# Performance work log

Hardware: AMD Instinct MI355X
Metric: run time of the kernel (lower is better)

Reference implementation:

```python
import jax, jax.numpy as jnp
import numpy as np

DIM = 512
NUM_HEADS = 8


def setup_inputs() -> dict:
    key = jax.random.key(0)
    ks = jax.random.split(key, 10)
    B, N, C = 2, 4096, DIM
    s = 0.02
    return {
        "x": jax.random.normal(ks[0], (B, N, C), dtype=jnp.float32),
        "Wq": jax.random.normal(ks[1], (C, C), dtype=jnp.float32) * s,
        "Wk": jax.random.normal(ks[2], (C, C), dtype=jnp.float32) * s,
        "Wv": jax.random.normal(ks[3], (C, C), dtype=jnp.float32) * s,
        "Wattn": jax.random.normal(ks[4], (C, C), dtype=jnp.float32) * s,
        "Wconv": jax.random.normal(ks[5], (C, C), dtype=jnp.float32) * s,
        "dw_kernel": jax.random.normal(ks[6], (C, 1, 3), dtype=jnp.float32) * s,  # depthwise (O, I/groups, K)
        "dw_bias": jax.random.normal(ks[7], (C,), dtype=jnp.float32) * s,
        "Wcout": jax.random.normal(ks[8], (C, C), dtype=jnp.float32) * s,
        "H": 8,
        "W": 512,
    }


def reference(x, Wq, Wk, Wv, Wattn, Wconv, dw_kernel, dw_bias, Wcout, H, W):
    B, N, C = x.shape
    nh = NUM_HEADS
    hd = C // nh
    scale = hd ** (-0.5)

    # QKV projections (torch Linear: x @ W.T), split heads -> [B, nh, N, hd]
    q = (x @ Wq.T).reshape(B, N, nh, hd).transpose(0, 2, 1, 3)
    k = (x @ Wk.T).reshape(B, N, nh, hd).transpose(0, 2, 1, 3)
    v = (x @ Wv.T).reshape(B, N, nh, hd).transpose(0, 2, 1, 3)

    # Materialized N x N attention (faithful to source)
    scores = jnp.einsum("bhqd,bhkd->bhqk", q, k) * scale
    weights = jax.nn.softmax(scores, axis=-1)
    attn = jnp.einsum("bhqk,bhkd->bhqd", weights, v)
    attn = attn.transpose(0, 2, 1, 3).reshape(B, N, C)
    attn_out = attn @ Wattn.T

    # Parallel depthwise-conv branch
    ci = (x @ Wconv.T).transpose(0, 2, 1)  # [B, C, N]
    co = jax.lax.conv_general_dilated(
        ci, dw_kernel,
        window_strides=(1,), padding=((1, 1),),
        feature_group_count=C,
        dimension_numbers=("NCH", "OIH", "NCH"),
    ) + dw_bias[None, :, None]
    conv_out = co.transpose(0, 2, 1) @ Wcout.T  # [B, N, C]

    out = attn_out + conv_out
    # NOTE: source shadows arg H with num_heads before the view
    return out.reshape(B, nh, W, C)
```

## Files before the change

kernel.cpp:

```cpp
#include <hip/hip_runtime.h>

typedef __attribute__((ext_vector_type(8))) short bf16x8;
typedef __attribute__((ext_vector_type(4))) float f32x4;

constexpr int kB = 2, kN = 4096, kC = 512, kNH = 8, kHD = 64;
constexpr int kBN = kB * kN;
constexpr int kWElems = 262144;
constexpr int kWAll = 6 * kWElems;
constexpr int kWExtra = 3584;
constexpr float kQScale = 0.1803368801f;

__device__ __forceinline__ short f2bf(float f) {
  union { float f; unsigned u; } v; v.f = f;
  unsigned r = v.u + 0x7fffu + ((v.u >> 16) & 1u);
  return (short)(r >> 16);
}
__device__ __forceinline__ float bf2f(short s) {
  union { unsigned u; float f; } v; v.u = ((unsigned)(unsigned short)s) << 16;
  return v.f;
}
__device__ __forceinline__ float exp2_(float x) {
#if __has_builtin(__builtin_amdgcn_exp2f)
  return __builtin_amdgcn_exp2f(x);
#else
  return exp2f(x);
#endif
}
__device__ __forceinline__ unsigned pk2bf(float a, float b) {
  union { float f; unsigned u; } ua, ub; ua.f = a; ub.f = b;
#if __has_builtin(__builtin_amdgcn_perm)
  return __builtin_amdgcn_perm(ub.u + 0x8000u, ua.u + 0x8000u, 0x07060302u);
#else
  return ((ua.u + 0x8000u) >> 16) | (((ub.u + 0x8000u) >> 16) << 16);
#endif
}

__device__ __forceinline__ bf16x8 ld8(const short* p) { return *(const bf16x8*)p; }
__device__ __forceinline__ bf16x8 ld8(const float* p) {
  float4 a = *(const float4*)p;
  float4 b = *(const float4*)(p + 4);
  bf16x8 r;
  r[0] = f2bf(a.x); r[1] = f2bf(a.y); r[2] = f2bf(a.z); r[3] = f2bf(a.w);
  r[4] = f2bf(b.x); r[5] = f2bf(b.y); r[6] = f2bf(b.z); r[7] = f2bf(b.w);
  return r;
}
__device__ __forceinline__ void stf(short* p, float v) { *p = f2bf(v); }
__device__ __forceinline__ void stf(float* p, float v) { *p = v; }

__device__ __forceinline__ void gload_lds16(const void* g, void* l) {
  __builtin_amdgcn_global_load_lds(
      (const __attribute__((address_space(1))) void*)g,
      (__attribute__((address_space(3))) void*)l, 16, 0, 0);
}

__global__ void detect_dtype(const unsigned* __restrict__ x, int* __restrict__ flag) {
  const int lane = threadIdx.x & 63;
  unsigned w = x[lane];
  int e = (int)((w >> 7) & 0xffu);
  bool bf = (e >= 100 && e <= 140);
  unsigned long long m = __ballot(bf);
  if (lane == 0) *flag = (__popcll(m) >= 32) ? 1 : 0;
}

constexpr int kW8 = kWAll / 8;
constexpr int kX8 = kBN * kC / 8;
__global__ __launch_bounds__(256) void convert_all(
    const void* Wq, const void* Wk, const void* Wv, const void* Wc,
    const void* Wa, const void* Wco, const void* dwk, const void* dwb,
    const void* x, const int* __restrict__ flag, short* __restrict__ dst,
    short* __restrict__ xb) {
  const int gtid = blockIdx.x * 256 + threadIdx.x;
  const bool bf = (*flag != 0);
  if (gtid < kW8) {
    const int e = gtid * 8;
    const int t = e >> 18, off = e & (kWElems - 1);
    const void* src = (t == 0) ? Wq : (t == 1) ? Wk : (t == 2) ? Wv
                    : (t == 3) ? Wc : (t == 4) ? Wa : Wco;
    bf16x8 v = bf ? ld8((const short*)src + off) : ld8((const float*)src + off);
    *(bf16x8*)(dst + e) = v;
  } else if (gtid < kW8 + kWExtra) {
    const int eoff = gtid - kW8;
    if (eoff < 1536) {
      dst[kWAll + eoff] = bf ? ((const short*)dwk)[eoff]
                             : f2bf(((const float*)dwk)[eoff]);
    } else if (eoff < 2048) {
      const int i = eoff - 1536;
      dst[kWAll + 1536 + i] = bf ? ((const short*)dwb)[i]
                                 : f2bf(((const float*)dwb)[i]);
    } else {
      const int t2 = eoff - 2048;
      const int tap = t2 >> 9, c = t2 & 511;
      dst[kWAll + 2048 + t2] = bf ? ((const short*)dwk)[c * 3 + tap]
                                  : f2bf(((const float*)dwk)[c * 3 + tap]);
    }
  } else if (gtid < kW8 + kWExtra + kX8) {
    const int e = (gtid - kW8 - kWExtra) * 8;
    bf16x8 v = bf ? ld8((const short*)x + e) : ld8((const float*)x + e);
    *(bf16x8*)(xb + e) = v;
  }
}

__global__ __launch_bounds__(256, 3) void proj_gemm(
    const short* __restrict__ xb, const short* __restrict__ wb,
    short* __restrict__ q, short* __restrict__ k, short* __restrict__ vT,
    short* __restrict__ ci) {
  __shared__ __align__(16) short As[128 * 64];
  __shared__ __align__(16) short Bs[128 * 64];
  const int t = threadIdx.x;
  const int wave = t >> 6, lane = t & 63;
  const int row = lane & 15, quad = lane >> 4;
  const int bn = blockIdx.x & 15;
  const int bm = blockIdx.x >> 4;
  const int m0 = bm * 128, n0 = bn * 128;
  const int wm = wave & 1, wn = wave >> 1;
  const int lrow = lane >> 3, lch = lane & 7;

  f32x4 acc[4][4];
#pragma unroll
  for (int mi = 0; mi < 4; ++mi)
#pragma unroll
    for (int ni = 0; ni < 4; ++ni)
#pragma unroll
      for (int r = 0; r < 4; ++r) acc[mi][ni][r] = 0.0f;

  for (int k0 = 0; k0 < kC; k0 += 64) {
#pragma unroll
    for (int p = 0; p < 4; ++p) {
      const int m = wave * 32 + p * 8 + lrow;
      const int kch = lch ^ (m & 7);
      gload_lds16(xb + (size_t)(m0 + m) * kC + k0 + kch * 8,
                  &As[(wave * 32 + p * 8) * 64]);
      gload_lds16(wb + (size_t)(n0 + m) * kC + k0 + kch * 8,
                  &Bs[(wave * 32 + p * 8) * 64]);
    }
    __syncthreads();

#pragma unroll
    for (int kk2 = 0; kk2 < 2; ++kk2) {
      bf16x8 af[4], bfr[4];
#pragma unroll
      for (int mi = 0; mi < 4; ++mi) {
        const int m = wm * 64 + mi * 16 + row;
        const int ch = (kk2 * 4 + quad) ^ (m & 7);
        af[mi] = *(const bf16x8*)(&As[m * 64 + ch * 8]);
      }
#pragma unroll
      for (int ni = 0; ni < 4; ++ni) {
        const int n = wn * 64 + ni * 16 + row;
        const int ch = (kk2 * 4 + quad) ^ (n & 7);
        bfr[ni] = *(const bf16x8*)(&Bs[n * 64 + ch * 8]);
      }
#pragma unroll
      for (int mi = 0; mi < 4; ++mi)
#pragma unroll
        for (int ni = 0; ni < 4; ++ni)
          acc[mi][ni] = __builtin_amdgcn_mfma_f32_16x16x32_bf16(
              af[mi], bfr[ni], acc[mi][ni], 0, 0, 0);
    }
    __syncthreads();
  }

  const int gc0 = n0 + wn * 64;
  const int mat = gc0 >> 9;
  const float scale = (mat == 0) ? kQScale : 1.0f;
#pragma unroll
  for (int mi = 0; mi < 4; ++mi) {
#pragma unroll
    for (int ni = 0; ni < 4; ++ni) {
#pragma unroll
      for (int r = 0; r < 4; ++r) {
        const int gm = m0 + wm * 64 + mi * 16 + quad * 4 + r;
        const int c_ = ((gc0 + ni * 16) & 511) + row;
        const int b_ = gm >> 12;
        const int n_ = gm & (kN - 1);
        const short bv = f2bf(acc[mi][ni][r] * scale);
        if (mat == 3) {
          ci[(b_ * kN + n_) * kC + c_] = bv;
        } else {
          const int h = c_ >> 6, d = c_ & 63;
          const int bh = b_ * kNH + h;
          if (mat == 0)      q[(bh * kN + n_) * kHD + d] = bv;
          else if (mat == 1) k[(bh * kN + n_) * kHD + d] = bv;
          else               vT[(bh * kHD + d) * kN + n_] = bv;
        }
      }
    }
  }
}

__global__ __launch_bounds__(256) void dwconv(
    const short* __restrict__ ci, const short* __restrict__ wb,
    short* __restrict__ cb) {
  const int e0 = (blockIdx.x * 256 + threadIdx.x) * 8;
  const int c0 = e0 & (kC - 1);
  const int bn = e0 >> 9;
  const int n_ = bn & (kN - 1);
  bf16x8 xc = ld8(ci + e0);
  bf16x8 xm, xp;
  if (n_ > 0) xm = ld8(ci + e0 - kC);
  else
#pragma unroll
    for (int i = 0; i < 8; ++i) xm[i] = 0;
  if (n_ < kN - 1) xp = ld8(ci + e0 + kC);
  else
#pragma unroll
    for (int i = 0; i < 8; ++i) xp[i] = 0;
  bf16x8 w0 = ld8(wb + kWAll + 2048 + c0);
  bf16x8 w1 = ld8(wb + kWAll + 2048 + 512 + c0);
  bf16x8 w2 = ld8(wb + kWAll + 2048 + 1024 + c0);
  bf16x8 bi = ld8(wb + kWAll + 1536 + c0);
  bf16x8 o;
#pragma unroll
  for (int i = 0; i < 8; ++i) {
    float a = bf2f(bi[i]) + bf2f(xm[i]) * bf2f(w0[i]) +
              bf2f(xc[i]) * bf2f(w1[i]) + bf2f(xp[i]) * bf2f(w2[i]);
    o[i] = f2bf(a);
  }
  *(bf16x8*)(cb + e0) = o;
}

__global__ __launch_bounds__(512, 4) void attn_flash(
    const short* __restrict__ q, const short* __restrict__ k,
    const short* __restrict__ vT, short* __restrict__ attn) {
  __shared__ __align__(16) short Kb[2][2][64 * 64];
  __shared__ __align__(16) short VbS[2][2][64 * 72];
  const int t = threadIdx.x;
  const int wave = t >> 6;
  const int lane = t & 63;
  const int row = lane & 15;
  const int quad = lane >> 4;
  const int qg = wave & 3;
  const int ks = wave >> 2;

  const int slot = blockIdx.x & 7;
  const int inner = blockIdx.x >> 3;
  const int bh = slot * 2 + (inner & 1);
  const int q0 = (inner >> 1) * 128 + qg * 32;

  const short* qbase = q + (size_t)(bh * kN + q0) * kHD;
  const short* kbase = k + (size_t)bh * kN * kHD;
  const short* vbase = vT + (size_t)bh * kHD * kN;

  bf16x8 qb[2][2];
#pragma unroll
  for (int g = 0; g < 2; ++g) {
    qb[g][0] = *(const bf16x8*)(qbase + (g * 16 + row) * kHD + quad * 8);
    qb[g][1] = *(const bf16x8*)(qbase + (g * 16 + row) * kHD + 32 + quad * 8);
  }

  f32x4 o[2][4];
#pragma unroll
  for (int g = 0; g < 2; ++g)
#pragma unroll
    for (int j = 0; j < 4; ++j)
#pragma unroll
      for (int r = 0; r < 4; ++r) o[g][j][r] = 0.0f;
  float l_[2] = {0.0f, 0.0f};

  const int ksrow = lane >> 3;
  const int kschunk = (lane & 7) ^ ksrow;
  auto stage_k = [&](int buf, int kt) {
#pragma unroll
    for (int s2 = 0; s2 < 2; ++s2)
      gload_lds16(
          kbase + (size_t)(s2 * 2048 + kt * 64 + wave * 8 + ksrow) * 64 +
              kschunk * 8,
          &Kb[buf][s2][wave * 512]);
  };

  const int sv = t >> 8;
  const int ii = t & 255;
  const int i0 = ii, i1 = ii + 256;
  const int sr0 = i0 >> 3, sc0 = i0 & 7;
  const int sr1 = i1 >> 3, sc1 = i1 & 7;
  const int vb0 = (sc0 >> 2) * 32 + (sc0 & 1) * 16 + (sc0 & 2) * 2;
  const int vb1 = (sc1 >> 2) * 32 + (sc1 & 1) * 16 + (sc1 & 2) * 2;

  auto stage_v = [&](int buf, bf16x8 v0, bf16x8 v1) {
    *(short4*)(&VbS[buf][sv][sr0 * 72 + vb0]) =
        make_short4(v0[0], v0[1], v0[2], v0[3]);
    *(short4*)(&VbS[buf][sv][sr0 * 72 + vb0 + 8]) =
        make_short4(v0[4], v0[5], v0[6], v0[7]);
    *(short4*)(&VbS[buf][sv][sr1 * 72 + vb1]) =
        make_short4(v1[0], v1[1], v1[2], v1[3]);
    *(short4*)(&VbS[buf][sv][sr1 * 72 + vb1 + 8]) =
        make_short4(v1[4], v1[5], v1[6], v1[7]);
  };

  const int c0s = ((quad) ^ (row & 7)) * 8;
  const int c1s = ((quad + 4) ^ (row & 7)) * 8;

  auto tile_step = [&](const short* kt_base, const short* vt_base) {
    f32x4 s[2][4];
#pragma unroll
    for (int g = 0; g < 2; ++g)
#pragma unroll
      for (int jk = 0; jk < 4; ++jk)
#pragma unroll
        for (int r = 0; r < 4; ++r) s[g][jk][r] = 0.0f;
    __builtin_amdgcn_s_setprio(1);
#pragma unroll
    for (int jk = 0; jk < 4; ++jk) {
      const short* kr = kt_base + (jk * 16 + row) * 64;
      bf16x8 a0 = *(const bf16x8*)(kr + c0s);
      bf16x8 a1 = *(const bf16x8*)(kr + c1s);
#pragma unroll
      for (int g = 0; g < 2; ++g) {
        s[g][jk] = __builtin_amdgcn_mfma_f32_16x16x32_bf16(a0, qb[g][0], s[g][jk], 0, 0, 0);
        s[g][jk] = __builtin_amdgcn_mfma_f32_16x16x32_bf16(a1, qb[g][1], s[g][jk], 0, 0, 0);
      }
    }
    __builtin_amdgcn_s_setprio(0);

    bf16x8 pb[2][2];
#pragma unroll
    for (int g = 0; g < 2; ++g) {
      float tj[4];
#pragma unroll
      for (int jk = 0; jk < 4; ++jk) {
#pragma unroll
        for (int r = 0; r < 4; ++r) s[g][jk][r] = exp2_(s[g][jk][r]);
        tj[jk] = (s[g][jk][0] + s[g][jk][1]) + (s[g][jk][2] + s[g][jk][3]);
      }
      l_[g] += (tj[0] + tj[1]) + (tj[2] + tj[3]);
#pragma unroll
      for (int c = 0; c < 2; ++c) {
        union { unsigned u[4]; bf16x8 v; } pu;
        pu.u[0] = pk2bf(s[g][2 * c][0], s[g][2 * c][1]);
        pu.u[1] = pk2bf(s[g][2 * c][2], s[g][2 * c][3]);
        pu.u[2] = pk2bf(s[g][2 * c + 1][0], s[g][2 * c + 1][1]);
        pu.u[3] = pk2bf(s[g][2 * c + 1][2], s[g][2 * c + 1][3]);
        pb[g][c] = pu.v;
      }
    }

    __builtin_amdgcn_s_setprio(1);
#pragma unroll
    for (int jd = 0; jd < 4; ++jd) {
      const short* vb = vt_base + (jd * 16 + row) * 72 + quad * 8;
#pragma unroll
      for (int c = 0; c < 2; ++c) {
        bf16x8 av = *(const bf16x8*)(vb + c * 32);
#pragma unroll
        for (int g = 0; g < 2; ++g)
          o[g][jd] = __builtin_amdgcn_mfma_f32_16x16x32_bf16(
              av, pb[g][c], o[g][jd], 0, 0, 0);
      }
    }
    __builtin_amdgcn_s_setprio(0);
  };

  {
    stage_k(0, 0);
    bf16x8 a = *(const bf16x8*)(vbase + (size_t)sr0 * kN + sv * 2048 + sc0 * 8);
    bf16x8 b = *(const bf16x8*)(vbase + (size_t)sr1 * kN + sv * 2048 + sc1 * 8);
    stage_v(0, a, b);
  }
  __syncthreads();

  for (int kt = 0; kt < 32; ++kt) {
    const int cur = kt & 1;
    const bool more = (kt < 31);
    bf16x8 vn0, vn1;
    if (more) {
      stage_k(1 - cur, kt + 1);
      const int off = sv * 2048 + (kt + 1) * 64;
      vn0 = *(const bf16x8*)(vbase + (size_t)sr0 * kN + off + sc0 * 8);
      vn1 = *(const bf16x8*)(vbase + (size_t)sr1 * kN + off + sc1 * 8);
    }

    tile_step(&Kb[cur][ks][0], &VbS[cur][ks][0]);

    if (more) stage_v(1 - cur, vn0, vn1);
    __syncthreads();
  }

  float* Of = (float*)&Kb[0][0][0];
  float* Lf = (float*)&VbS[0][0][0];
  if (ks == 1) {
#pragma unroll
    for (int g = 0; g < 2; ++g) {
#pragma unroll
      for (int jd = 0; jd < 4; ++jd)
#pragma unroll
        for (int r = 0; r < 4; ++r)
          Of[(g * 16 + jd * 4 + r) * 256 + qg * 64 + lane] = o[g][jd][r];
      Lf[g * 256 + qg * 64 + lane] = l_[g];
    }
  }
  __syncthreads();
  if (ks == 0) {
#pragma unroll
    for (int g = 0; g < 2; ++g) {
#pragma unroll
      for (int jd = 0; jd < 4; ++jd)
#pragma unroll
        for (int r = 0; r < 4; ++r)
          o[g][jd][r] += Of[(g * 16 + jd * 4 + r) * 256 + qg * 64 + lane];
      l_[g] += Lf[g * 256 + qg * 64 + lane];
    }
    const int b_ = bh >> 3, h = bh & 7;
#pragma unroll
    for (int g = 0; g < 2; ++g) {
      float lt = l_[g];
      lt += __shfl_xor(lt, 16);
      lt += __shfl_xor(lt, 32);
      const float linv = 1.0f / lt;
      const int n_ = q0 + g * 16 + row;
      short* ob = attn + (size_t)(b_ * kN + n_) * kC + h * kHD + quad * 4;
#pragma unroll
      for (int jd = 0; jd < 4; ++jd) {
        short4 st = make_short4(f2bf(o[g][jd][0] * linv), f2bf(o[g][jd][1] * linv),
                                f2bf(o[g][jd][2] * linv), f2bf(o[g][jd][3] * linv));
        *(short4*)(ob + jd * 16) = st;
      }
    }
  }
}

template <typename TO>
__device__ __forceinline__ void out_body(
    const short* __restrict__ attn, const short* __restrict__ cb,
    const short* __restrict__ wb, TO* __restrict__ out) {
  __shared__ __align__(16) short As[128 * 64];
  __shared__ __align__(16) short Bs[64 * 64];
  const int t = threadIdx.x;
  const int wave = t >> 6, lane = t & 63;
  const int row = lane & 15, quad = lane >> 4;
  const int bn = blockIdx.x & 7;
  const int bm = blockIdx.x >> 3;
  const int m0 = bm * 128, n0 = bn * 64;
  const int wm = wave & 1, wn = wave >> 1;
  const int lrow = lane >> 3, lch = lane & 7;

  f32x4 acc[4][2];
#pragma unroll
  for (int mi = 0; mi < 4; ++mi)
#pragma unroll
    for (int ni = 0; ni < 2; ++ni)
#pragma unroll
      for (int r = 0; r < 4; ++r) acc[mi][ni][r] = 0.0f;

  const short* Wa = wb + 4 * kWElems;
  const short* Wo = wb + 5 * kWElems;

  for (int k0 = 0; k0 < 1024; k0 += 64) {
    const short* Asrc = (k0 < 512) ? attn : cb;
    const short* Bsrc = (k0 < 512) ? Wa : Wo;
    const int ka = k0 & 511;
#pragma unroll
    for (int p = 0; p < 4; ++p) {
      const int m = wave * 32 + p * 8 + lrow;
      const int kch = lch ^ (m & 7);
      gload_lds16(Asrc + (size_t)(m0 + m) * kC + ka + kch * 8,
                  &As[(wave * 32 + p * 8) * 64]);
    }
#pragma unroll
    for (int p = 0; p < 2; ++p) {
      const int n = wave * 16 + p * 8 + lrow;
      const int kch = lch ^ (n & 7);
      gload_lds16(Bsrc + (size_t)(n0 + n) * kC + ka + kch * 8,
                  &Bs[(wave * 16 + p * 8) * 64]);
    }
    __syncthreads();

#pragma unroll
    for (int kk2 = 0; kk2 < 2; ++kk2) {
      bf16x8 af[4], bfr[2];
#pragma unroll
      for (int mi = 0; mi < 4; ++mi) {
        const int m = wm * 64 + mi * 16 + row;
        const int ch = (kk2 * 4 + quad) ^ (m & 7);
        af[mi] = *(const bf16x8*)(&As[m * 64 + ch * 8]);
      }
#pragma unroll
      for (int ni = 0; ni < 2; ++ni) {
        const int n = wn * 32 + ni * 16 + row;
        const int ch = (kk2 * 4 + quad) ^ (n & 7);
        bfr[ni] = *(const bf16x8*)(&Bs[n * 64 + ch * 8]);
      }
#pragma unroll
      for (int mi = 0; mi < 4; ++mi)
#pragma unroll
        for (int ni = 0; ni < 2; ++ni)
          acc[mi][ni] = __builtin_amdgcn_mfma_f32_16x16x32_bf16(
              af[mi], bfr[ni], acc[mi][ni], 0, 0, 0);
    }
    __syncthreads();
  }

#pragma unroll
  for (int mi = 0; mi < 4; ++mi)
#pragma unroll
    for (int ni = 0; ni < 2; ++ni)
#pragma unroll
      for (int r = 0; r < 4; ++r) {
        const int gm = m0 + wm * 64 + mi * 16 + quad * 4 + r;
        const int gc = n0 + wn * 32 + ni * 16 + row;
        stf(out + (size_t)gm * kC + gc, acc[mi][ni][r]);
      }
}

__global__ __launch_bounds__(256, 4) void out_gemm(
    const short* __restrict__ attn, const short* __restrict__ cb,
    const short* __restrict__ wb, const int* __restrict__ flag, void* out) {
  if (*flag)
    out_body<short>(attn, cb, wb, (short*)out);
  else
    out_body<float>(attn, cb, wb, (float*)out);
}

extern "C" void kernel_launch(void* const* d_in, const int* in_sizes, int n_in,
                              void* d_out, int out_size, void* d_ws, size_t ws_size,
                              hipStream_t stream) {
  const void* x   = d_in[0];
  const void* Wq  = d_in[1];
  const void* Wk  = d_in[2];
  const void* Wv  = d_in[3];
  const void* Wa  = d_in[4];
  const void* Wc  = d_in[5];
  const void* dwk = d_in[6];
  const void* dwb = d_in[7];
  const void* Wco = d_in[8];

  short* ws = (short*)d_ws;
  const size_t E = (size_t)kBN * kC;
  int*   flag = (int*)ws;
  short* wb   = ws + 256;
  short* q    = wb + kWAll + kWExtra;
  short* k    = q + E;
  short* vT   = k + E;
  short* ci   = vT + E;
  short* cb   = ci + E;
  short* attn = ci;
  short* xb   = cb;

  detect_dtype<<<1, 64, 0, stream>>>((const unsigned*)x, flag);
  const int cvt_threads = kW8 + kWExtra + kX8;
  convert_all<<<(cvt_threads + 255) / 256, 256, 0, stream>>>(
      Wq, Wk, Wv, Wc, Wa, Wco, dwk, dwb, x, flag, wb, xb);
  proj_gemm<<<1024, 256, 0, stream>>>(xb, wb, q, k, vT, ci);
  dwconv<<<(kBN * kC) / (256 * 8), 256, 0, stream>>>(ci, wb, cb);
  attn_flash<<<512, 512, 0, stream>>>(q, k, vT, attn);
  out_gemm<<<512, 256, 0, stream>>>(attn, cb, wb, flag, d_out);
}
```

Before: 245.8 us.

## Stage GEMM epilogues through swizzled LDS for coalesced vector stores

The projection and output GEMM epilogues now write accumulators into a shared-memory tile with an XOR swizzle, then read rows back and emit 16-byte vectorized global stores. Before, each thread scattered scalar 2- or 4-byte stores. The V-projection tile is transposed in LDS so the vT layout can also be written with wide stores. The attention kernel also feeds a zero vector directly into the first MFMA instead of zero-initialising the score accumulators. The cost is an extra barrier and LDS round trip per block, plus reuse of the A/B tile buffers for staging.

```diff
diff --git a/kernel.cpp b/kernel.cpp
--- a/kernel.cpp
+++ b/kernel.cpp
@@ -44,8 +44,6 @@
   r[4] = f2bf(b.x); r[5] = f2bf(b.y); r[6] = f2bf(b.z); r[7] = f2bf(b.w);
   return r;
 }
-__device__ __forceinline__ void stf(short* p, float v) { *p = f2bf(v); }
-__device__ __forceinline__ void stf(float* p, float v) { *p = v; }
 
 __device__ __forceinline__ void gload_lds16(const void* g, void* l) {
   __builtin_amdgcn_global_load_lds(
@@ -104,8 +102,9 @@
     const short* __restrict__ xb, const short* __restrict__ wb,
     short* __restrict__ q, short* __restrict__ k, short* __restrict__ vT,
     short* __restrict__ ci) {
-  __shared__ __align__(16) short As[128 * 64];
-  __shared__ __align__(16) short Bs[128 * 64];
+  __shared__ __align__(16) short Sh[16384];
+  short* As = Sh;
+  short* Bs = Sh + 8192;
   const int t = threadIdx.x;
   const int wave = t >> 6, lane = t & 63;
   const int row = lane & 15, quad = lane >> 4;
@@ -160,29 +159,54 @@
     __syncthreads();
   }
 
-  const int gc0 = n0 + wn * 64;
-  const int mat = gc0 >> 9;
+  const int mat = n0 >> 9;
   const float scale = (mat == 0) ? kQScale : 1.0f;
-#pragma unroll
-  for (int mi = 0; mi < 4; ++mi) {
-#pragma unroll
-    for (int ni = 0; ni < 4; ++ni) {
-#pragma unroll
-      for (int r = 0; r < 4; ++r) {
-        const int gm = m0 + wm * 64 + mi * 16 + quad * 4 + r;
-        const int c_ = ((gc0 + ni * 16) & 511) + row;
-        const int b_ = gm >> 12;
-        const int n_ = gm & (kN - 1);
-        const short bv = f2bf(acc[mi][ni][r] * scale);
-        if (mat == 3) {
-          ci[(b_ * kN + n_) * kC + c_] = bv;
-        } else {
-          const int h = c_ >> 6, d = c_ & 63;
-          const int bh = b_ * kNH + h;
-          if (mat == 0)      q[(bh * kN + n_) * kHD + d] = bv;
-          else if (mat == 1) k[(bh * kN + n_) * kHD + d] = bv;
-          else               vT[(bh * kHD + d) * kN + n_] = bv;
+  if (mat != 2) {
+#pragma unroll
+    for (int mi = 0; mi < 4; ++mi)
+#pragma unroll
+      for (int ni = 0; ni < 4; ++ni)
+#pragma unroll
+        for (int r = 0; r < 4; ++r) {
+          const int m = wm * 64 + mi * 16 + quad * 4 + r;
+          const int n = wn * 64 + ni * 16 + row;
+          Sh[m * 128 + (((n >> 3) ^ (m & 15)) * 8) + (n & 7)] =
+              f2bf(acc[mi][ni][r] * scale);
         }
+  } else {
+#pragma unroll
+    for (int mi = 0; mi < 4; ++mi)
+#pragma unroll
+      for (int ni = 0; ni < 4; ++ni)
+#pragma unroll
+        for (int r = 0; r < 4; ++r) {
+          const int m = wm * 64 + mi * 16 + quad * 4 + r;
+          const int n = wn * 64 + ni * 16 + row;
+          Sh[n * 128 + (((m >> 3) ^ (n & 15)) * 8) + (m & 7)] =
+              f2bf(acc[mi][ni][r]);
+        }
+  }
+  __syncthreads();
+  const int b_ = m0 >> 12;
+  const int rsub = lane >> 4, chk = lane & 15;
+#pragma unroll
+  for (int i = 0; i < 8; ++i) {
+    const int rr = i * 16 + wave * 4 + rsub;
+    bf16x8 v = *(const bf16x8*)(&Sh[rr * 128 + ((chk ^ (rr & 15)) * 8)]);
+    if (mat == 2) {
+      const int cg = (n0 + rr) & 511;
+      const int h = cg >> 6, d = cg & 63;
+      const int nb = (m0 & (kN - 1)) + chk * 8;
+      *(bf16x8*)(vT + ((size_t)((b_ * kNH + h) * kHD + d)) * kN + nb) = v;
+    } else {
+      const int n_ = (m0 & (kN - 1)) + rr;
+      const int cg = (n0 + chk * 8) & 511;
+      if (mat == 3) {
+        *(bf16x8*)(ci + ((size_t)(b_ * kN + n_)) * kC + cg) = v;
+      } else {
+        const int h = cg >> 6, d = cg & 63;
+        short* dst = (mat == 0) ? q : k;
+        *(bf16x8*)(dst + ((size_t)((b_ * kNH + h) * kN + n_)) * kHD + d) = v;
       }
     }
   }
@@ -248,6 +272,8 @@
     qb[g][1] = *(const bf16x8*)(qbase + (g * 16 + row) * kHD + 32 + quad * 8);
   }
 
+  const f32x4 z4 = {0.0f, 0.0f, 0.0f, 0.0f};
+
   f32x4 o[2][4];
 #pragma unroll
   for (int g = 0; g < 2; ++g)
@@ -292,12 +318,6 @@
 
   auto tile_step = [&](const short* kt_base, const short* vt_base) {
     f32x4 s[2][4];
-#pragma unroll
-    for (int g = 0; g < 2; ++g)
-#pragma unroll
-      for (int jk = 0; jk < 4; ++jk)
-#pragma unroll
-        for (int r = 0; r < 4; ++r) s[g][jk][r] = 0.0f;
     __builtin_amdgcn_s_setprio(1);
 #pragma unroll
     for (int jk = 0; jk < 4; ++jk) {
@@ -306,7 +326,7 @@
       bf16x8 a1 = *(const bf16x8*)(kr + c1s);
 #pragma unroll
       for (int g = 0; g < 2; ++g) {
-        s[g][jk] = __builtin_amdgcn_mfma_f32_16x16x32_bf16(a0, qb[g][0], s[g][jk], 0, 0, 0);
+        s[g][jk] = __builtin_amdgcn_mfma_f32_16x16x32_bf16(a0, qb[g][0], z4, 0, 0, 0);
         s[g][jk] = __builtin_amdgcn_mfma_f32_16x16x32_bf16(a1, qb[g][1], s[g][jk], 0, 0, 0);
       }
     }
@@ -422,8 +442,9 @@
 __device__ __forceinline__ void out_body(
     const short* __restrict__ attn, const short* __restrict__ cb,
     const short* __restrict__ wb, TO* __restrict__ out) {
-  __shared__ __align__(16) short As[128 * 64];
-  __shared__ __align__(16) short Bs[64 * 64];
+  __shared__ __align__(16) short Sh[16384];
+  short* As = Sh;
+  short* Bs = Sh + 8192;
   const int t = threadIdx.x;
   const int wave = t >> 6, lane = t & 63;
   const int row = lane & 15, quad = lane >> 4;
@@ -489,16 +510,47 @@
     __syncthreads();
   }
 
-#pragma unroll
-  for (int mi = 0; mi < 4; ++mi)
-#pragma unroll
-    for (int ni = 0; ni < 2; ++ni)
-#pragma unroll
-      for (int r = 0; r < 4; ++r) {
-        const int gm = m0 + wm * 64 + mi * 16 + quad * 4 + r;
-        const int gc = n0 + wn * 32 + ni * 16 + row;
-        stf(out + (size_t)gm * kC + gc, acc[mi][ni][r]);
-      }
+  if constexpr (sizeof(TO) == 4) {
+    float* Shf = (float*)Sh;
+#pragma unroll
+    for (int mi = 0; mi < 4; ++mi)
+#pragma unroll
+      for (int ni = 0; ni < 2; ++ni)
+#pragma unroll
+        for (int r = 0; r < 4; ++r) {
+          const int m = wm * 64 + mi * 16 + quad * 4 + r;
+          const int n = wn * 32 + ni * 16 + row;
+          Shf[m * 64 + (((n >> 2) ^ (m & 15)) * 4) + (n & 3)] = acc[mi][ni][r];
+        }
+    __syncthreads();
+    const int rsub = lane >> 4, chk = lane & 15;
+#pragma unroll
+    for (int i = 0; i < 8; ++i) {
+      const int rr = i * 16 + wave * 4 + rsub;
+      float4 v = *(const float4*)(&Shf[rr * 64 + ((chk ^ (rr & 15)) * 4)]);
+      *(float4*)((float*)out + (size_t)(m0 + rr) * kC + n0 + chk * 4) = v;
+    }
+  } else {
+#pragma unroll
+    for (int mi = 0; mi < 4; ++mi)
+#pragma unroll
+      for (int ni = 0; ni < 2; ++ni)
+#pragma unroll
+        for (int r = 0; r < 4; ++r) {
+          const int m = wm * 64 + mi * 16 + quad * 4 + r;
+          const int n = wn * 32 + ni * 16 + row;
+          Sh[m * 64 + (((n >> 3) ^ (m & 7)) * 8) + (n & 7)] =
+              f2bf(acc[mi][ni][r]);
+        }
+    __syncthreads();
+    const int rsub = lane >> 3, chk = lane & 7;
+#pragma unroll
+    for (int i = 0; i < 4; ++i) {
+      const int rr = i * 32 + wave * 8 + rsub;
+      bf16x8 v = *(const bf16x8*)(&Sh[rr * 64 + ((chk ^ (rr & 7)) * 8)]);
+      *(bf16x8*)((short*)out + (size_t)(m0 + rr) * kC + n0 + chk * 8) = v;
+    }
+  }
 }
 
 __global__ __launch_bounds__(256, 4) void out_gemm(
```

Result: faster. 222.6 us (-9.5%).
